# Kernel optimization log

Measured on AMD Instinct MI355X. Metric: run time of the kernel, lower is better.

Reference implementation:

```python
import jax, jax.numpy as jnp
import numpy as np

LAMBDA_TEMP = 20.0
GAMMA = 20.0
MARGIN = 0.05
EPS = 1e-8

B, K, M, D = 128, 256, 8, 128


def _unit(x, axis=-1):
    return x / jnp.linalg.norm(x, axis=axis, keepdims=True)


def setup_inputs() -> dict:
    key = jax.random.key(0)
    k1, k2, k3 = jax.random.split(key, 3)
    v_proj = _unit(jax.random.normal(k1, (B, K, D), dtype=jnp.float32))
    prototypes = _unit(jax.random.normal(k2, (K, M, D), dtype=jnp.float32))
    concept_labels = jax.random.randint(k3, (B, K), 0, 2, dtype=jnp.int64)
    return {"v_proj": v_proj, "concept_labels": concept_labels, "prototypes": prototypes}


def reference(v_proj, concept_labels, prototypes):
    # all-pairs prototype similarities: query vector (b,k) vs prototypes of concept c
    # sims: (B, K, C, M)
    sims = jnp.einsum('bkd,cmd->bkcm', v_proj, prototypes)
    # Eq.6: soft assignment over the M prototypes of each concept
    q = jax.nn.softmax(GAMMA * sims, axis=-1)
    # Eq.7-8: weighted similarity sim_c(v)  -> (B, K, C)
    sim = jnp.sum(q * sims, axis=-1)
    # positive similarity: concept k queried against its own prototypes, plus margin
    sim_pos = jnp.einsum('bkk->bk', sim) + MARGIN  # (B, K)
    # Eq.9: -log( exp(lam*sim_pos) / (sum_c exp(lam*sim_c) + eps) )
    denom = jnp.sum(jnp.exp(LAMBDA_TEMP * sim), axis=-1) + EPS  # (B, K)
    loss_bk = jnp.log(denom) - LAMBDA_TEMP * sim_pos  # (B, K)
    mask = (concept_labels == 1).astype(loss_bk.dtype)
    num_pos = jnp.sum(mask)
    total = jnp.sum(loss_bk * mask)
    return jnp.where(num_pos > 0, total / num_pos, total)
```

## Files before the change

### kernel.cpp

```cpp
#include <hip/hip_runtime.h>

#define LT      20.0f
#define LN2     0.69314718055994531f
#define C2EXP   28.853900817779268f
#define CHUNKS  16
#define NBLK    512
#define PW_COPY 262144

typedef _Float16 half8 __attribute__((ext_vector_type(8)));
typedef float    f32x4 __attribute__((ext_vector_type(4)));

#if __has_builtin(__builtin_amdgcn_exp2f)
#define EXP2F(x) __builtin_amdgcn_exp2f(x)
#else
#define EXP2F(x) __expf(0.69314718055994531f * (x))
#endif

__device__ __forceinline__ float swz16(float x) {
    return __int_as_float(__builtin_amdgcn_ds_swizzle(__float_as_int(x), 0x401F));
}

#define GLD16(gp, lp) __builtin_amdgcn_global_load_lds( \
    (const __attribute__((address_space(1))) void*)(gp), \
    (__attribute__((address_space(3))) void*)(lp), 16, 0, 0)

__global__ __launch_bounds__(256)
void mpcl_prep(const float* __restrict__ P, _Float16* __restrict__ Pw)
{
    int copy = blockIdx.x & 7;
    int id   = (blockIdx.x >> 3) * 256 + threadIdx.x;
    int ch    = id >> 11;
    int colq  = (id >> 9) & 3;
    int cfrag = (id >> 6) & 7;
    int lane  = id & 63;
    int n = lane & 15, q = lane >> 4;
    int c = cfrag & 3, h = cfrag >> 2;
    int col  = colq * 32 + ((n >> 2) << 3) + (n & 3) + (h << 2);
    int gcol = (ch << 7) + col;
    const float* src = P + ((size_t)gcol << 7) + c * 32 + q * 8;
    float4 a = *(const float4*)src;
    float4 b = *(const float4*)(src + 4);
    half8 hv;
    hv[0] = (_Float16)(C2EXP * a.x); hv[1] = (_Float16)(C2EXP * a.y);
    hv[2] = (_Float16)(C2EXP * a.z); hv[3] = (_Float16)(C2EXP * a.w);
    hv[4] = (_Float16)(C2EXP * b.x); hv[5] = (_Float16)(C2EXP * b.y);
    hv[6] = (_Float16)(C2EXP * b.z); hv[7] = (_Float16)(C2EXP * b.w);
    *(half8*)(Pw + (size_t)copy * PW_COPY + (size_t)id * 8) = hv;
}

__global__ __attribute__((amdgpu_flat_work_group_size(512, 512),
                          amdgpu_waves_per_eu(4, 4)))
void mpcl_main(const float* __restrict__ V,
               const int*   __restrict__ labels,
               const _Float16* __restrict__ Pw,
               float* __restrict__ part)
{
    __shared__ __align__(16) _Float16 Pst[2][2048 * 8];
    __shared__ float sh_denom[64];
    __shared__ float sh_simpos[64];

    const int tid  = threadIdx.x;
    const int lane = tid & 63;
    const int w    = tid >> 6;
    const int colq = w & 3;
    const int rg   = w >> 2;
    const int n    = lane & 15;
    const int q    = lane >> 4;
    const int rowbase = blockIdx.x * 64;

    if (tid < 64) { sh_denom[tid] = 0.0f; sh_simpos[tid] = 0.0f; }

    int lab = 0;
    if (tid < 64) lab = labels[rowbase + tid];

    const _Float16* gbase = Pw + (size_t)(blockIdx.x & 7) * PW_COPY
                               + (size_t)(w * 256 + lane) * 8;

#define STAGE(CH, B) do {                                       \
    const _Float16* g_ = gbase + (size_t)(CH) * 16384;          \
    _Float16* l_ = &Pst[B][(w * 256) * 8];                      \
    GLD16(g_,        l_);                                       \
    GLD16(g_ +  512, l_ +  512);                                \
    GLD16(g_ + 1024, l_ + 1024);                                \
    GLD16(g_ + 1536, l_ + 1536);                                \
} while (0)

    half8 vh[2][4];
#pragma unroll
    for (int rf = 0; rf < 2; ++rf) {
        const float* vr = V + ((size_t)(rowbase + rg * 32 + rf * 16 + n) << 7) + q * 8;
#pragma unroll
        for (int c = 0; c < 4; ++c) {
            float4 x0 = *(const float4*)(vr + c * 32);
            float4 x1 = *(const float4*)(vr + c * 32 + 4);
            vh[rf][c][0] = (_Float16)x0.x; vh[rf][c][1] = (_Float16)x0.y;
            vh[rf][c][2] = (_Float16)x0.z; vh[rf][c][3] = (_Float16)x0.w;
            vh[rf][c][4] = (_Float16)x1.x; vh[rf][c][5] = (_Float16)x1.y;
            vh[rf][c][6] = (_Float16)x1.z; vh[rf][c][7] = (_Float16)x1.w;
        }
    }

    __syncthreads();

    STAGE(0, 0);
    STAGE(1, 1);

    const int rowk0 = (rowbase + rg * 32 + n) & 255;
    const int rowk1 = (rowbase + rg * 32 + 16 + n) & 255;
    const int aoff  = (colq * 512 + lane) * 8;

    float dn0 = 0.f, dn1 = 0.f;
    int cA = colq * 4 + q;

#pragma unroll 1
    for (int ch = 0; ch < CHUNKS; ++ch) {
        if (ch < CHUNKS - 1) asm volatile("s_waitcnt vmcnt(4)" ::: "memory");
        else                 asm volatile("s_waitcnt vmcnt(0)" ::: "memory");
        __builtin_amdgcn_s_barrier();

        const _Float16* base = &Pst[ch & 1][0];

        f32x4 acc1[2] = {{0.f,0.f,0.f,0.f},{0.f,0.f,0.f,0.f}};
        f32x4 acc2[2] = {{0.f,0.f,0.f,0.f},{0.f,0.f,0.f,0.f}};
#pragma unroll
        for (int c = 0; c < 4; ++c) {
            half8 a1 = *(const half8*)&base[aoff + c * 512];
            half8 a2 = *(const half8*)&base[aoff + c * 512 + 2048];
            acc1[0] = __builtin_amdgcn_mfma_f32_16x16x32_f16(a1, vh[0][c], acc1[0], 0, 0, 0);
            acc1[1] = __builtin_amdgcn_mfma_f32_16x16x32_f16(a1, vh[1][c], acc1[1], 0, 0, 0);
            acc2[0] = __builtin_amdgcn_mfma_f32_16x16x32_f16(a2, vh[0][c], acc2[0], 0, 0, 0);
            acc2[1] = __builtin_amdgcn_mfma_f32_16x16x32_f16(a2, vh[1][c], acc2[1], 0, 0, 0);
        }

#pragma unroll
        for (int rf = 0; rf < 2; ++rf) {
            float x0 = acc1[rf][0], x1 = acc1[rf][1], x2 = acc1[rf][2], x3 = acc1[rf][3];
            float x4 = acc2[rf][0], x5 = acc2[rf][1], x6 = acc2[rf][2], x7 = acc2[rf][3];
            float e0 = EXP2F(x0), e1 = EXP2F(x1), e2 = EXP2F(x2), e3 = EXP2F(x3);
            float e4 = EXP2F(x4), e5 = EXP2F(x5), e6 = EXP2F(x6), e7 = EXP2F(x7);
            float es = ((e0 + e1) + (e2 + e3)) + ((e4 + e5) + (e6 + e7));
            float ss = fmaf(e0, x0, fmaf(e1, x1, fmaf(e2, x2, e3 * x3)))
                     + fmaf(e4, x4, fmaf(e5, x5, fmaf(e6, x6, e7 * x7)));
            float simY = __fdividef(ss, es);
            if (rf) dn1 += EXP2F(simY); else dn0 += EXP2F(simY);
            if (cA == (rf ? rowk1 : rowk0))
                sh_simpos[rg * 32 + rf * 16 + n] = simY;
        }
        cA += 16;

        __builtin_amdgcn_s_barrier();
        if (ch + 2 < CHUNKS) STAGE(ch + 2, ch & 1);
    }

#pragma unroll
    for (int rf = 0; rf < 2; ++rf) {
        float t = rf ? dn1 : dn0;
        t += swz16(t);
        t += __shfl_xor(t, 32);
        if (lane < 16)
            atomicAdd(&sh_denom[rg * 32 + rf * 16 + n], t);
    }
    __syncthreads();

    float s = 0.f, cc = 0.f;
    if (tid < 64) {
        float lp = logf(sh_denom[tid] + 1e-8f) - LN2 * sh_simpos[tid] - 1.0f;
        float mk = (lab == 1) ? 1.0f : 0.0f;
        s = lp * mk;
        cc = mk;
    }
#pragma unroll
    for (int off = 32; off >= 1; off >>= 1) {
        s  += __shfl_down(s, off);
        cc += __shfl_down(cc, off);
    }

    if (tid == 0) {
        part[2 * blockIdx.x]     = s;
        part[2 * blockIdx.x + 1] = cc;
    }
}

__global__ __launch_bounds__(512)
void mpcl_finish(const float* __restrict__ part, float* __restrict__ out)
{
    __shared__ float sh[16];
    const int tid  = threadIdx.x;
    const int lane = tid & 63;
    const int w    = tid >> 6;

    float s  = part[2 * tid];
    float cc = part[2 * tid + 1];
#pragma unroll
    for (int off = 32; off >= 1; off >>= 1) {
        s  += __shfl_down(s, off);
        cc += __shfl_down(cc, off);
    }
    if (lane == 0) { sh[w] = s; sh[8 + w] = cc; }
    __syncthreads();
    if (tid == 0) {
        float ts = 0.f, tc = 0.f;
#pragma unroll
        for (int i = 0; i < 8; ++i) { ts += sh[i]; tc += sh[8 + i]; }
        out[0] = (tc > 0.0f) ? (ts / tc) : ts;
    }
}

extern "C" void kernel_launch(void* const* d_in, const int* in_sizes, int n_in,
                              void* d_out, int out_size, void* d_ws, size_t ws_size,
                              hipStream_t stream)
{
    const float* V      = (const float*)d_in[0];
    const int*   labels = (const int*)d_in[1];
    const float* P      = (const float*)d_in[2];
    float* out  = (float*)d_out;
    float* part = (float*)d_ws;
    _Float16* Pw = (_Float16*)((char*)d_ws + 16384);

    mpcl_prep<<<1024, 256, 0, stream>>>(P, Pw);
    mpcl_main<<<NBLK, 512, 0, stream>>>(V, labels, Pw, part);
    mpcl_finish<<<1, 512, 0, stream>>>(part, out);
}
```

Baseline: 99.12 us.

## Use 1024-thread blocks with one row fragment per wave and a single prototype copy

The main kernel now runs 16 waves per block, each owning one 16-row fragment instead of two, which halves per-wave MFMA and register work while keeping 64 rows per block. The prep kernel writes one swizzled fp16 prototype copy instead of eight, using coalesced reads of the source. The next-chunk LDS stage is issued right after the MFMAs (with an lgkmcnt wait and barrier) so the softmax epilogue overlaps the loads. The trade-offs are more waves contending for the same LDS and barriers, and all blocks reading the same global copy.

```diff
diff --git a/kernel.cpp b/kernel.cpp
--- a/kernel.cpp
+++ b/kernel.cpp
@@ -5,7 +5,6 @@
 #define C2EXP   28.853900817779268f
 #define CHUNKS  16
 #define NBLK    512
-#define PW_COPY 262144
 
 typedef _Float16 half8 __attribute__((ext_vector_type(8)));
 typedef float    f32x4 __attribute__((ext_vector_type(4)));
@@ -27,29 +26,31 @@
 __global__ __launch_bounds__(256)
 void mpcl_prep(const float* __restrict__ P, _Float16* __restrict__ Pw)
 {
-    int copy = blockIdx.x & 7;
-    int id   = (blockIdx.x >> 3) * 256 + threadIdx.x;
-    int ch    = id >> 11;
-    int colq  = (id >> 9) & 3;
-    int cfrag = (id >> 6) & 7;
-    int lane  = id & 63;
-    int n = lane & 15, q = lane >> 4;
-    int c = cfrag & 3, h = cfrag >> 2;
-    int col  = colq * 32 + ((n >> 2) << 3) + (n & 3) + (h << 2);
-    int gcol = (ch << 7) + col;
-    const float* src = P + ((size_t)gcol << 7) + c * 32 + q * 8;
+    int t    = blockIdx.x * 256 + threadIdx.x;
+    int gcol = t >> 4;
+    int dblk = t & 15;
+    const float* src = P + ((size_t)gcol << 7) + dblk * 8;
     float4 a = *(const float4*)src;
     float4 b = *(const float4*)(src + 4);
+
+    int ch   = gcol >> 7, col  = gcol & 127;
+    int colq = col >> 5,  col5 = col & 31;
+    int g = col5 >> 3, p = col5 & 7;
+    int n = (g << 2) | (p & 3), h = p >> 2;
+    int c = dblk >> 2, q = dblk & 3;
+    int lane  = (q << 4) | n;
+    int cfrag = (h << 2) | c;
+    int slot  = ch * 2048 + colq * 512 + cfrag * 64 + lane;
+
     half8 hv;
     hv[0] = (_Float16)(C2EXP * a.x); hv[1] = (_Float16)(C2EXP * a.y);
     hv[2] = (_Float16)(C2EXP * a.z); hv[3] = (_Float16)(C2EXP * a.w);
     hv[4] = (_Float16)(C2EXP * b.x); hv[5] = (_Float16)(C2EXP * b.y);
     hv[6] = (_Float16)(C2EXP * b.z); hv[7] = (_Float16)(C2EXP * b.w);
-    *(half8*)(Pw + (size_t)copy * PW_COPY + (size_t)id * 8) = hv;
-}
-
-__global__ __attribute__((amdgpu_flat_work_group_size(512, 512),
-                          amdgpu_waves_per_eu(4, 4)))
+    *(half8*)(Pw + (size_t)slot * 8) = hv;
+}
+
+__global__ __launch_bounds__(1024, 8)
 void mpcl_main(const float* __restrict__ V,
                const int*   __restrict__ labels,
                const _Float16* __restrict__ Pw,
@@ -73,111 +74,100 @@
     int lab = 0;
     if (tid < 64) lab = labels[rowbase + tid];
 
-    const _Float16* gbase = Pw + (size_t)(blockIdx.x & 7) * PW_COPY
-                               + (size_t)(w * 256 + lane) * 8;
+    const _Float16* gbase = Pw + (size_t)(w * 128 + lane) * 8;
 
 #define STAGE(CH, B) do {                                       \
     const _Float16* g_ = gbase + (size_t)(CH) * 16384;          \
-    _Float16* l_ = &Pst[B][(w * 256) * 8];                      \
-    GLD16(g_,        l_);                                       \
-    GLD16(g_ +  512, l_ +  512);                                \
-    GLD16(g_ + 1024, l_ + 1024);                                \
-    GLD16(g_ + 1536, l_ + 1536);                                \
+    _Float16* l_ = &Pst[B][(w * 128) * 8];                      \
+    GLD16(g_,       l_);                                        \
+    GLD16(g_ + 512, l_ + 512);                                  \
 } while (0)
 
-    half8 vh[2][4];
-#pragma unroll
-    for (int rf = 0; rf < 2; ++rf) {
-        const float* vr = V + ((size_t)(rowbase + rg * 32 + rf * 16 + n) << 7) + q * 8;
+    half8 vh[4];
+    {
+        const float* vr = V + ((size_t)(rowbase + rg * 16 + n) << 7) + q * 8;
 #pragma unroll
         for (int c = 0; c < 4; ++c) {
             float4 x0 = *(const float4*)(vr + c * 32);
             float4 x1 = *(const float4*)(vr + c * 32 + 4);
-            vh[rf][c][0] = (_Float16)x0.x; vh[rf][c][1] = (_Float16)x0.y;
-            vh[rf][c][2] = (_Float16)x0.z; vh[rf][c][3] = (_Float16)x0.w;
-            vh[rf][c][4] = (_Float16)x1.x; vh[rf][c][5] = (_Float16)x1.y;
-            vh[rf][c][6] = (_Float16)x1.z; vh[rf][c][7] = (_Float16)x1.w;
-        }
-    }
-
+            vh[c][0] = (_Float16)x0.x; vh[c][1] = (_Float16)x0.y;
+            vh[c][2] = (_Float16)x0.z; vh[c][3] = (_Float16)x0.w;
+            vh[c][4] = (_Float16)x1.x; vh[c][5] = (_Float16)x1.y;
+            vh[c][6] = (_Float16)x1.z; vh[c][7] = (_Float16)x1.w;
+        }
+    }
     __syncthreads();
 
     STAGE(0, 0);
     STAGE(1, 1);
 
-    const int rowk0 = (rowbase + rg * 32 + n) & 255;
-    const int rowk1 = (rowbase + rg * 32 + 16 + n) & 255;
-    const int aoff  = (colq * 512 + lane) * 8;
-
-    float dn0 = 0.f, dn1 = 0.f;
+    const int rowk = (rowbase + rg * 16 + n) & 255;
+    const int aoff = (colq * 512 + lane) * 8;
+
+    float dn = 0.f;
     int cA = colq * 4 + q;
 
 #pragma unroll 1
     for (int ch = 0; ch < CHUNKS; ++ch) {
-        if (ch < CHUNKS - 1) asm volatile("s_waitcnt vmcnt(4)" ::: "memory");
+        if (ch < CHUNKS - 1) asm volatile("s_waitcnt vmcnt(2)" ::: "memory");
         else                 asm volatile("s_waitcnt vmcnt(0)" ::: "memory");
         __builtin_amdgcn_s_barrier();
 
         const _Float16* base = &Pst[ch & 1][0];
 
-        f32x4 acc1[2] = {{0.f,0.f,0.f,0.f},{0.f,0.f,0.f,0.f}};
-        f32x4 acc2[2] = {{0.f,0.f,0.f,0.f},{0.f,0.f,0.f,0.f}};
+        f32x4 acc1 = {0.f, 0.f, 0.f, 0.f};
+        f32x4 acc2 = {0.f, 0.f, 0.f, 0.f};
 #pragma unroll
         for (int c = 0; c < 4; ++c) {
             half8 a1 = *(const half8*)&base[aoff + c * 512];
             half8 a2 = *(const half8*)&base[aoff + c * 512 + 2048];
-            acc1[0] = __builtin_amdgcn_mfma_f32_16x16x32_f16(a1, vh[0][c], acc1[0], 0, 0, 0);
-            acc1[1] = __builtin_amdgcn_mfma_f32_16x16x32_f16(a1, vh[1][c], acc1[1], 0, 0, 0);
-            acc2[0] = __builtin_amdgcn_mfma_f32_16x16x32_f16(a2, vh[0][c], acc2[0], 0, 0, 0);
-            acc2[1] = __builtin_amdgcn_mfma_f32_16x16x32_f16(a2, vh[1][c], acc2[1], 0, 0, 0);
-        }
-
-#pragma unroll
-        for (int rf = 0; rf < 2; ++rf) {
-            float x0 = acc1[rf][0], x1 = acc1[rf][1], x2 = acc1[rf][2], x3 = acc1[rf][3];
-            float x4 = acc2[rf][0], x5 = acc2[rf][1], x6 = acc2[rf][2], x7 = acc2[rf][3];
+            acc1 = __builtin_amdgcn_mfma_f32_16x16x32_f16(a1, vh[c], acc1, 0, 0, 0);
+            acc2 = __builtin_amdgcn_mfma_f32_16x16x32_f16(a2, vh[c], acc2, 0, 0, 0);
+        }
+
+        asm volatile("s_waitcnt lgkmcnt(0)" ::: "memory");
+        __builtin_amdgcn_s_barrier();
+        if (ch + 2 < CHUNKS) STAGE(ch + 2, ch & 1);
+
+        {
+            float x0 = acc1[0], x1 = acc1[1], x2 = acc1[2], x3 = acc1[3];
+            float x4 = acc2[0], x5 = acc2[1], x6 = acc2[2], x7 = acc2[3];
             float e0 = EXP2F(x0), e1 = EXP2F(x1), e2 = EXP2F(x2), e3 = EXP2F(x3);
             float e4 = EXP2F(x4), e5 = EXP2F(x5), e6 = EXP2F(x6), e7 = EXP2F(x7);
             float es = ((e0 + e1) + (e2 + e3)) + ((e4 + e5) + (e6 + e7));
             float ss = fmaf(e0, x0, fmaf(e1, x1, fmaf(e2, x2, e3 * x3)))
                      + fmaf(e4, x4, fmaf(e5, x5, fmaf(e6, x6, e7 * x7)));
             float simY = __fdividef(ss, es);
-            if (rf) dn1 += EXP2F(simY); else dn0 += EXP2F(simY);
-            if (cA == (rf ? rowk1 : rowk0))
-                sh_simpos[rg * 32 + rf * 16 + n] = simY;
+            dn += EXP2F(simY);
+            if (cA == rowk)
+                sh_simpos[rg * 16 + n] = simY;
         }
         cA += 16;
-
-        __builtin_amdgcn_s_barrier();
-        if (ch + 2 < CHUNKS) STAGE(ch + 2, ch & 1);
-    }
-
-#pragma unroll
-    for (int rf = 0; rf < 2; ++rf) {
-        float t = rf ? dn1 : dn0;
+    }
+
+    {
+        float t = dn;
         t += swz16(t);
         t += __shfl_xor(t, 32);
         if (lane < 16)
-            atomicAdd(&sh_denom[rg * 32 + rf * 16 + n], t);
+            atomicAdd(&sh_denom[rg * 16 + n], t);
     }
     __syncthreads();
 
-    float s = 0.f, cc = 0.f;
-    if (tid < 64) {
-        float lp = logf(sh_denom[tid] + 1e-8f) - LN2 * sh_simpos[tid] - 1.0f;
+    if (w == 0) {
+        float lp = logf(sh_denom[lane] + 1e-8f) - LN2 * sh_simpos[lane] - 1.0f;
         float mk = (lab == 1) ? 1.0f : 0.0f;
-        s = lp * mk;
-        cc = mk;
-    }
-#pragma unroll
-    for (int off = 32; off >= 1; off >>= 1) {
-        s  += __shfl_down(s, off);
-        cc += __shfl_down(cc, off);
-    }
-
-    if (tid == 0) {
-        part[2 * blockIdx.x]     = s;
-        part[2 * blockIdx.x + 1] = cc;
+        float s  = lp * mk;
+        float cc = mk;
+#pragma unroll
+        for (int off = 32; off >= 1; off >>= 1) {
+            s  += __shfl_down(s, off);
+            cc += __shfl_down(cc, off);
+        }
+        if (lane == 0) {
+            part[2 * blockIdx.x]     = s;
+            part[2 * blockIdx.x + 1] = cc;
+        }
     }
 }
 
@@ -217,7 +207,7 @@
     float* part = (float*)d_ws;
     _Float16* Pw = (_Float16*)((char*)d_ws + 16384);
 
-    mpcl_prep<<<1024, 256, 0, stream>>>(P, Pw);
-    mpcl_main<<<NBLK, 512, 0, stream>>>(V, labels, Pw, part);
+    mpcl_prep<<<128, 256, 0, stream>>>(P, Pw);
+    mpcl_main<<<NBLK, 1024, 0, stream>>>(V, labels, Pw, part);
     mpcl_finish<<<1, 512, 0, stream>>>(part, out);
 }
```

Result: no change. 97.21 us (-1.9%).
